# Kernel optimization log

Hardware: AMD Instinct MI355X
Metric: run time of the kernel (lower is better)

## Reference

```python
import jax, jax.numpy as jnp
import numpy as np

B, CAP, H, NH = 128, 65536, 512, 8
HD = H // NH
GH = H // 4  # gate hidden


def setup_inputs() -> dict:
    key = jax.random.key(0)
    ks = jax.random.split(key, 8)
    s = 1.0 / np.sqrt(H)
    sg = 1.0 / np.sqrt(GH)
    return {
        "query": jax.random.normal(ks[0], (B, H), jnp.float32),
        "memory_keys": jax.random.normal(ks[1], (CAP, H), jnp.float32) * s,
        "memory_values": jax.random.normal(ks[2], (CAP, H), jnp.float32) * s,
        "in_proj_w": jax.random.normal(ks[3], (3 * H, H), jnp.float32) * s,
        "in_proj_b": jnp.zeros((3 * H,), jnp.float32),
        "out_proj_w": jax.random.normal(ks[4], (H, H), jnp.float32) * s,
        "out_proj_b": jnp.zeros((H,), jnp.float32),
        "gate_w1": jax.random.normal(ks[5], (GH, H), jnp.float32) * s,
        "gate_b1": jnp.zeros((GH,), jnp.float32),
        "gate_w2": jax.random.normal(ks[6], (1, GH), jnp.float32) * sg,
        "gate_b2": jnp.zeros((1,), jnp.float32),
        "usage_count": jnp.zeros((CAP,), jnp.float32),
        "last_used": jnp.zeros((CAP,), jnp.float32),
        "step_counter": 1,
    }


def reference(query, memory_keys, memory_values, in_proj_w, in_proj_b,
              out_proj_w, out_proj_b, gate_w1, gate_b1, gate_w2, gate_b2,
              usage_count, last_used, step_counter):
    # nn.MultiheadAttention packed projections: rows [0:H]=Wq, [H:2H]=Wk, [2H:3H]=Wv
    wq, wk, wv = in_proj_w[:H], in_proj_w[H:2 * H], in_proj_w[2 * H:]
    bq, bk, bv = in_proj_b[:H], in_proj_b[H:2 * H], in_proj_b[2 * H:]

    q = (query @ wq.T + bq).reshape(B, NH, HD)           # [B, h, d] (q_len = 1)
    k = (memory_keys @ wk.T + bk).reshape(CAP, NH, HD)   # [C, h, d]
    v = (memory_values @ wv.T + bv).reshape(CAP, NH, HD)  # [C, h, d]

    scores = jnp.einsum('bhd,chd->bhc', q, k) / np.sqrt(HD)  # [B, h, C]
    attn = jax.nn.softmax(scores, axis=-1)
    ctx = jnp.einsum('bhc,chd->bhd', attn, v).reshape(B, H)
    attn_out = ctx @ out_proj_w.T + out_proj_b               # [B, H]

    # usage bookkeeping: attn_weights averaged over heads, then over batch
    avg_attn = attn.mean(axis=(0, 1))                        # [C]
    new_usage = usage_count + avg_attn
    new_last = jnp.where(avg_attn > 1e-3,
                         jnp.float32(step_counter), last_used)

    # gating MLP: Linear -> ReLU -> Linear -> Sigmoid
    gate = jax.nn.sigmoid(
        jax.nn.relu(query @ gate_w1.T + gate_b1) @ gate_w2.T + gate_b2)  # [B, 1]
    memory_output = gate * attn_out                          # [B, H]
    return memory_output, new_usage, new_last
```

## Files before the change

kernel.cpp:

```cpp
#include <hip/hip_runtime.h>
#include <stdint.h>


typedef __bf16 b16x8 __attribute__((ext_vector_type(8)));
typedef float f32x4 __attribute__((ext_vector_type(4)));

static __device__ __forceinline__ unsigned short f2bf(float f) {
  return __builtin_bit_cast(unsigned short, (__bf16)f);
}

static __device__ __forceinline__ f32x4 MFMA(b16x8 a, b16x8 b, f32x4 c) {
  return __builtin_amdgcn_mfma_f32_16x16x32_bf16(a, b, c, 0, 0, 0);
}

#define GLL16(g, l)                                                          \
  __builtin_amdgcn_global_load_lds(                                          \
      (const __attribute__((address_space(1))) void*)(g),                    \
      (__attribute__((address_space(3))) void*)(l), 16, 0, 0)

#define SBAR() __builtin_amdgcn_sched_barrier(0)

__global__ void k_convert_w(const float* __restrict__ w, unsigned short* __restrict__ dst) {
  int i = blockIdx.x * 256 + threadIdx.x;
  float4 v = reinterpret_cast<const float4*>(w + 512 * 512)[i];
  ushort4 o;
  o.x = f2bf(v.x); o.y = f2bf(v.y); o.z = f2bf(v.z); o.w = f2bf(v.w);
  reinterpret_cast<ushort4*>(dst)[i] = o;
}

__global__ void k_proj_q(const float* __restrict__ query, const float* __restrict__ w,
                         const float* __restrict__ bias, unsigned short* __restrict__ qout) {
  __shared__ float qs[512];
  int b = blockIdx.x, j = threadIdx.x;
  qs[j] = query[b * 512 + j];
  __syncthreads();
  float acc = bias[j];
  const float4* q4 = reinterpret_cast<const float4*>(qs);
  const float4* w4 = reinterpret_cast<const float4*>(w + j * 512);
#pragma unroll 8
  for (int i = 0; i < 128; ++i) {
    float4 a = q4[i], c = w4[i];
    acc += a.x * c.x + a.y * c.y + a.z * c.z + a.w * c.w;
  }
  qout[b * 512 + j] = f2bf(acc);
}

__global__ void k_gate(const float* __restrict__ query, const float* __restrict__ w1,
                       const float* __restrict__ b1, const float* __restrict__ w2,
                       const float* __restrict__ b2, float* __restrict__ gate) {
  __shared__ float qs[512];
  __shared__ float red[2];
  int b = blockIdx.x, j = threadIdx.x;
  qs[j] = query[b * 512 + j];
  qs[j + 128] = query[b * 512 + j + 128];
  qs[j + 256] = query[b * 512 + j + 256];
  qs[j + 384] = query[b * 512 + j + 384];
  __syncthreads();
  float acc = b1[j];
  const float4* q4 = reinterpret_cast<const float4*>(qs);
  const float4* w4 = reinterpret_cast<const float4*>(w1 + j * 512);
#pragma unroll 8
  for (int i = 0; i < 128; ++i) {
    float4 a = q4[i], c = w4[i];
    acc += a.x * c.x + a.y * c.y + a.z * c.z + a.w * c.w;
  }
  float t = fmaxf(acc, 0.f) * w2[j];
#pragma unroll
  for (int off = 1; off < 64; off <<= 1) t += __shfl_xor(t, off, 64);
  if ((j & 63) == 0) red[j >> 6] = t;
  __syncthreads();
  if (j == 0) {
    float z = red[0] + red[1] + b2[0];
    gate[b] = 1.f / (1.f + __builtin_amdgcn_exp2f(-z * 1.44269504088896f));
  }
}

__global__ __launch_bounds__(512, 4) void k_proj_kv(
    const float* __restrict__ mk, const float* __restrict__ mv,
    const unsigned short* __restrict__ wkb, const unsigned short* __restrict__ wvb,
    const float* __restrict__ in_b,
    unsigned short* __restrict__ kout, unsigned short* __restrict__ vtout) {
  const int p = blockIdx.x;
  const int xcd = p & 7, slot = p >> 3;
  const int isV = xcd >> 2;
  const int j0 = (slot & 3) * 128;
  const int c0 = (xcd & 3) * 16384 + (slot >> 2) * 128;
  const float* Ag = isV ? mv : mk;
  const unsigned short* W = isV ? wvb : wkb;
  const float* bias = in_b + (isV ? 1024 : 512);
  const int tid = threadIdx.x;
  const int w = tid >> 6, wr = w >> 2, wc = w & 3;
  const int ln = tid & 15, g = (tid & 63) >> 4;
  const int sw = (ln >> 1) & 3;

  __shared__ __align__(16) unsigned short Al[2][128 * 32];
  __shared__ __align__(16) unsigned short Wl[2][128 * 32];

  f32x4 acc[4][2];
#pragma unroll
  for (int m = 0; m < 4; ++m)
#pragma unroll
    for (int n = 0; n < 2; ++n) acc[m][n] = {0.f, 0.f, 0.f, 0.f};

  const int arow = tid >> 2, aq = tid & 3;
  const float* aptr = Ag + (size_t)(c0 + arow) * 512 + aq * 8;
  const int aoff = arow * 32 + ((aq ^ ((arow >> 1) & 3)) << 3);

  const int lane = tid & 63;
  const int wrow = 16 * w + (lane >> 2);
  const int wps = (lane & 3) ^ ((wrow >> 1) & 3);
  const unsigned short* wsrc = W + (size_t)(j0 + wrow) * 512 + wps * 8;
  const int wdoff = w * 512;

  float4 aA0, aA1, aB0, aB1;

  GLL16(wsrc, &Wl[0][wdoff]);
  SBAR();
  {
    const float4* ap = reinterpret_cast<const float4*>(aptr);
    aA0 = ap[0]; aA1 = ap[1];
  }
  SBAR();
  asm volatile("s_waitcnt vmcnt(0)" ::: "memory");
  SBAR();
  {
    b16x8 v;
    v[0] = (__bf16)aA0.x; v[1] = (__bf16)aA0.y; v[2] = (__bf16)aA0.z; v[3] = (__bf16)aA0.w;
    v[4] = (__bf16)aA1.x; v[5] = (__bf16)aA1.y; v[6] = (__bf16)aA1.z; v[7] = (__bf16)aA1.w;
    *reinterpret_cast<b16x8*>(&Al[0][aoff]) = v;
  }
  {
    const float4* ap = reinterpret_cast<const float4*>(aptr + 32);
    aB0 = ap[0]; aB1 = ap[1];
  }
  SBAR();
  asm volatile("s_waitcnt lgkmcnt(0)" ::: "memory");
  SBAR();
  __builtin_amdgcn_s_barrier();

#pragma unroll 2
  for (int kk = 0; kk < 16; ++kk) {
    const int cur = kk & 1, nxt = cur ^ 1;
    b16x8 af[4], wf[2];
#pragma unroll
    for (int m = 0; m < 4; ++m) {
      int row = 64 * wr + 16 * m + ln;
      af[m] = *reinterpret_cast<const b16x8*>(&Al[cur][row * 32 + ((g ^ sw) << 3)]);
    }
#pragma unroll
    for (int n = 0; n < 2; ++n) {
      int row = 32 * wc + 16 * n + ln;
      wf[n] = *reinterpret_cast<const b16x8*>(&Wl[cur][row * 32 + ((g ^ sw) << 3)]);
    }
    const int k1 = (kk < 15) ? kk + 1 : 15;
    GLL16(wsrc + k1 * 32, &Wl[nxt][wdoff]);
    SBAR();
    const int k2 = (kk < 14) ? kk + 2 : 15;
    {
      const float4* ap = reinterpret_cast<const float4*>(aptr + k2 * 32);
      if (cur == 0) { aA0 = ap[0]; aA1 = ap[1]; }
      else          { aB0 = ap[0]; aB1 = ap[1]; }
    }
    SBAR();
    if (!isV) {
#pragma unroll
      for (int m = 0; m < 4; ++m)
#pragma unroll
        for (int n = 0; n < 2; ++n) acc[m][n] = MFMA(wf[n], af[m], acc[m][n]);
    } else {
#pragma unroll
      for (int m = 0; m < 4; ++m)
#pragma unroll
        for (int n = 0; n < 2; ++n) acc[m][n] = MFMA(af[m], wf[n], acc[m][n]);
    }
    SBAR();
    asm volatile("s_waitcnt vmcnt(3)" ::: "memory");
    SBAR();
    {
      float4 f0 = (nxt == 0) ? aA0 : aB0, f1 = (nxt == 0) ? aA1 : aB1;
      b16x8 v;
      v[0] = (__bf16)f0.x; v[1] = (__bf16)f0.y; v[2] = (__bf16)f0.z; v[3] = (__bf16)f0.w;
      v[4] = (__bf16)f1.x; v[5] = (__bf16)f1.y; v[6] = (__bf16)f1.z; v[7] = (__bf16)f1.w;
      *reinterpret_cast<b16x8*>(&Al[nxt][aoff]) = v;
    }
    SBAR();
    asm volatile("s_waitcnt vmcnt(2) lgkmcnt(0)" ::: "memory");
    SBAR();
    __builtin_amdgcn_s_barrier();
  }

  if (!isV) {
#pragma unroll
    for (int m = 0; m < 4; ++m) {
      int c = c0 + 64 * wr + 16 * m + ln;
#pragma unroll
      for (int n = 0; n < 2; ++n) {
        int jb = j0 + 32 * wc + 16 * n + 4 * g;
        float4 bb = *reinterpret_cast<const float4*>(&bias[jb]);
        ushort4 o;
        o.x = f2bf(acc[m][n][0] + bb.x);
        o.y = f2bf(acc[m][n][1] + bb.y);
        o.z = f2bf(acc[m][n][2] + bb.z);
        o.w = f2bf(acc[m][n][3] + bb.w);
        *reinterpret_cast<ushort4*>(&kout[(size_t)c * 512 + jb]) = o;
      }
    }
  } else {
#pragma unroll
    for (int n = 0; n < 2; ++n) {
      int j = j0 + 32 * wc + 16 * n + ln;
      float bj = bias[j];
#pragma unroll
      for (int m = 0; m < 4; ++m) {
        int cb = c0 + 64 * wr + 16 * m + 4 * g;
        ushort4 o;
        o.x = f2bf(acc[m][n][0] + bj);
        o.y = f2bf(acc[m][n][1] + bj);
        o.z = f2bf(acc[m][n][2] + bj);
        o.w = f2bf(acc[m][n][3] + bj);
        *reinterpret_cast<ushort4*>(&vtout[(size_t)j * 65536 + cb]) = o;
      }
    }
  }
}

__global__ __launch_bounds__(256) void k_attn1(
    const unsigned short* __restrict__ kb, const unsigned short* __restrict__ vt,
    const unsigned short* __restrict__ qb,
    float* __restrict__ l_ws, float* __restrict__ ctxT) {
  const int h = blockIdx.y, cg = blockIdx.x;
  const int tid = threadIdx.x;
  const int wv = tid >> 6, wr = wv >> 1, wc = wv & 1;
  const int ln = tid & 15, g = (tid & 63) >> 4;
  __shared__ __align__(16) unsigned short kS[128 * 64];
  __shared__ __align__(16) unsigned short pS[128 * 128];
  __shared__ __align__(16) unsigned short vS[64 * 128];
  const float SC = 0.125f * 1.44269504088896f;

  b16x8 qf[4][2];
#pragma unroll
  for (int n = 0; n < 4; ++n)
#pragma unroll
    for (int ks = 0; ks < 2; ++ks) {
      int b = 64 * wc + 16 * n + ln;
      qf[n][ks] = *reinterpret_cast<const b16x8*>(&qb[(size_t)b * 512 + h * 64 + ks * 32 + g * 8]);
    }
  f32x4 pacc[2][4];
#pragma unroll
  for (int m = 0; m < 2; ++m)
#pragma unroll
    for (int n = 0; n < 4; ++n) pacc[m][n] = {0.f, 0.f, 0.f, 0.f};
  float lsum[4] = {0.f, 0.f, 0.f, 0.f};

  for (int it = 0; it < 8; ++it) {
    int c0g = cg * 1024 + it * 128;
#pragma unroll
    for (int i = 0; i < 4; ++i) {
      int fl = i * 256 + tid, row = fl >> 3, p8 = fl & 7;
      uint4 d = *reinterpret_cast<const uint4*>(&kb[(size_t)(c0g + row) * 512 + h * 64 + p8 * 8]);
      *reinterpret_cast<uint4*>(&kS[(row * 8 + (p8 ^ (row & 7))) * 8]) = d;
    }
#pragma unroll
    for (int i = 0; i < 4; ++i) {
      int fl = i * 256 + tid, row = fl >> 4, p16 = fl & 15;
      uint4 d = *reinterpret_cast<const uint4*>(&vt[(size_t)(h * 64 + row) * 65536 + c0g + p16 * 8]);
      *reinterpret_cast<uint4*>(&vS[(row * 16 + (p16 ^ (row & 7))) * 8]) = d;
    }
    __syncthreads();

    f32x4 sacc[4][4];
#pragma unroll
    for (int m = 0; m < 4; ++m)
#pragma unroll
      for (int n = 0; n < 4; ++n) sacc[m][n] = {0.f, 0.f, 0.f, 0.f};
#pragma unroll
    for (int ks = 0; ks < 2; ++ks) {
      b16x8 a[4];
#pragma unroll
      for (int m = 0; m < 4; ++m) {
        int row = 64 * wr + 16 * m + ln;
        a[m] = *reinterpret_cast<const b16x8*>(&kS[(row * 8 + ((ks * 4 + g) ^ (row & 7))) * 8]);
      }
#pragma unroll
      for (int m = 0; m < 4; ++m)
#pragma unroll
        for (int n = 0; n < 4; ++n) sacc[m][n] = MFMA(a[m], qf[n][ks], sacc[m][n]);
    }
#pragma unroll
    for (int m = 0; m < 4; ++m)
#pragma unroll
      for (int n = 0; n < 4; ++n) {
        float p0 = __builtin_amdgcn_exp2f(sacc[m][n][0] * SC);
        float p1 = __builtin_amdgcn_exp2f(sacc[m][n][1] * SC);
        float p2 = __builtin_amdgcn_exp2f(sacc[m][n][2] * SC);
        float p3 = __builtin_amdgcn_exp2f(sacc[m][n][3] * SC);
        lsum[n] += (p0 + p1) + (p2 + p3);
        int b = 64 * wc + 16 * n + ln;
        int c = 64 * wr + 16 * m + 4 * g;
        int base = b * 128 + (((c >> 3) ^ (b & 7)) * 8) + (c & 7);
        ushort2 lo, hi;
        lo.x = f2bf(p0); lo.y = f2bf(p1);
        hi.x = f2bf(p2); hi.y = f2bf(p3);
        *reinterpret_cast<ushort2*>(&pS[base]) = lo;
        *reinterpret_cast<ushort2*>(&pS[base + 2]) = hi;
      }
    __syncthreads();
#pragma unroll
    for (int ks = 0; ks < 4; ++ks) {
      b16x8 av[2], bp[4];
#pragma unroll
      for (int m = 0; m < 2; ++m) {
        int row = 32 * wr + 16 * m + ln;
        av[m] = *reinterpret_cast<const b16x8*>(&vS[(row * 16 + ((ks * 4 + g) ^ (row & 7))) * 8]);
      }
#pragma unroll
      for (int n = 0; n < 4; ++n) {
        int row = 64 * wc + 16 * n + ln;
        bp[n] = *reinterpret_cast<const b16x8*>(&pS[(row * 16 + ((ks * 4 + g) ^ (row & 7))) * 8]);
      }
#pragma unroll
      for (int m = 0; m < 2; ++m)
#pragma unroll
        for (int n = 0; n < 4; ++n) pacc[m][n] = MFMA(av[m], bp[n], pacc[m][n]);
    }
    __syncthreads();
  }
#pragma unroll
  for (int n = 0; n < 4; ++n) {
    float v = lsum[n];
    v += __shfl_xor(v, 16, 64);
    v += __shfl_xor(v, 32, 64);
    if ((tid & 63) < 16) atomicAdd(&l_ws[h * 128 + 64 * wc + 16 * n + ln], v);
  }
#pragma unroll
  for (int m = 0; m < 2; ++m)
#pragma unroll
    for (int n = 0; n < 4; ++n)
#pragma unroll
      for (int r = 0; r < 4; ++r) {
        int d = 32 * wr + 16 * m + 4 * g + r;
        int b = 64 * wc + 16 * n + ln;
        atomicAdd(&ctxT[(h * 64 + d) * 128 + b], pacc[m][n][r]);
      }
}

__global__ __launch_bounds__(256) void k_attn2(
    const unsigned short* __restrict__ kb, const unsigned short* __restrict__ qb,
    const float* __restrict__ l_ws, float* __restrict__ avgA) {
  const int h = blockIdx.y, cg = blockIdx.x;
  const int tid = threadIdx.x;
  const int wv = tid >> 6, wr = wv >> 1, wc = wv & 1;
  const int ln = tid & 15, g = (tid & 63) >> 4;
  __shared__ __align__(16) unsigned short kS[128 * 64];
  __shared__ float wS[128];
  const float SC = 0.125f * 1.44269504088896f;
  if (tid < 128) wS[tid] = 1.f / l_ws[h * 128 + tid];
  b16x8 qf[4][2];
#pragma unroll
  for (int n = 0; n < 4; ++n)
#pragma unroll
    for (int ks = 0; ks < 2; ++ks) {
      int b = 64 * wc + 16 * n + ln;
      qf[n][ks] = *reinterpret_cast<const b16x8*>(&qb[(size_t)b * 512 + h * 64 + ks * 32 + g * 8]);
    }
  __syncthreads();
  float wn[4];
#pragma unroll
  for (int n = 0; n < 4; ++n) wn[n] = wS[64 * wc + 16 * n + ln];

  for (int it = 0; it < 8; ++it) {
    int c0g = cg * 1024 + it * 128;
#pragma unroll
    for (int i = 0; i < 4; ++i) {
      int fl = i * 256 + tid, row = fl >> 3, p8 = fl & 7;
      uint4 d = *reinterpret_cast<const uint4*>(&kb[(size_t)(c0g + row) * 512 + h * 64 + p8 * 8]);
      *reinterpret_cast<uint4*>(&kS[(row * 8 + (p8 ^ (row & 7))) * 8]) = d;
    }
    __syncthreads();
    f32x4 sacc[4][4];
#pragma unroll
    for (int m = 0; m < 4; ++m)
#pragma unroll
      for (int n = 0; n < 4; ++n) sacc[m][n] = {0.f, 0.f, 0.f, 0.f};
#pragma unroll
    for (int ks = 0; ks < 2; ++ks) {
      b16x8 a[4];
#pragma unroll
      for (int m = 0; m < 4; ++m) {
        int row = 64 * wr + 16 * m + ln;
        a[m] = *reinterpret_cast<const b16x8*>(&kS[(row * 8 + ((ks * 4 + g) ^ (row & 7))) * 8]);
      }
#pragma unroll
      for (int m = 0; m < 4; ++m)
#pragma unroll
        for (int n = 0; n < 4; ++n) sacc[m][n] = MFMA(a[m], qf[n][ks], sacc[m][n]);
    }
#pragma unroll
    for (int m = 0; m < 4; ++m) {
      float s0 = 0.f, s1 = 0.f, s2 = 0.f, s3 = 0.f;
#pragma unroll
      for (int n = 0; n < 4; ++n) {
        s0 += __builtin_amdgcn_exp2f(sacc[m][n][0] * SC) * wn[n];
        s1 += __builtin_amdgcn_exp2f(sacc[m][n][1] * SC) * wn[n];
        s2 += __builtin_amdgcn_exp2f(sacc[m][n][2] * SC) * wn[n];
        s3 += __builtin_amdgcn_exp2f(sacc[m][n][3] * SC) * wn[n];
      }
#pragma unroll
      for (int off = 1; off < 16; off <<= 1) {
        s0 += __shfl_xor(s0, off, 64);
        s1 += __shfl_xor(s1, off, 64);
        s2 += __shfl_xor(s2, off, 64);
        s3 += __shfl_xor(s3, off, 64);
      }
      if (ln == 0) {
        int c = c0g + 64 * wr + 16 * m + 4 * g;
        atomicAdd(&avgA[c], s0);
        atomicAdd(&avgA[c + 1], s1);
        atomicAdd(&avgA[c + 2], s2);
        atomicAdd(&avgA[c + 3], s3);
      }
    }
    __syncthreads();
  }
}

__global__ void k_finalize(const float* __restrict__ ctxT, const float* __restrict__ l_ws,
                           const float* __restrict__ wout, const float* __restrict__ bout,
                           const float* __restrict__ gate, float* __restrict__ out) {
  __shared__ float cs[512];
  int b = blockIdx.x, j = threadIdx.x;
  cs[j] = ctxT[j * 128 + b] / l_ws[(j >> 6) * 128 + b];
  __syncthreads();
  float acc = bout[j];
  const float4* c4 = reinterpret_cast<const float4*>(cs);
  const float4* w4 = reinterpret_cast<const float4*>(wout + j * 512);
#pragma unroll 8
  for (int i = 0; i < 128; ++i) {
    float4 a = c4[i], c = w4[i];
    acc += a.x * c.x + a.y * c.y + a.z * c.z + a.w * c.w;
  }
  out[b * 512 + j] = gate[b] * acc;
}

__global__ void k_usage(const float* __restrict__ avgA, const float* __restrict__ usage,
                        const float* __restrict__ last, const int* __restrict__ step,
                        float* __restrict__ out_usage, float* __restrict__ out_last) {
  int c = blockIdx.x * 256 + threadIdx.x;
  float avg = avgA[c] * (1.f / 1024.f);
  out_usage[c] = usage[c] + avg;
  out_last[c] = (avg > 0.001f) ? (float)step[0] : last[c];
}

extern "C" void kernel_launch(void* const* d_in, const int* in_sizes, int n_in,
                              void* d_out, int out_size, void* d_ws, size_t ws_size,
                              hipStream_t stream) {
  const float* query = (const float*)d_in[0];
  const float* mk    = (const float*)d_in[1];
  const float* mv    = (const float*)d_in[2];
  const float* in_w  = (const float*)d_in[3];
  const float* in_b  = (const float*)d_in[4];
  const float* out_w = (const float*)d_in[5];
  const float* out_b = (const float*)d_in[6];
  const float* gw1   = (const float*)d_in[7];
  const float* gb1   = (const float*)d_in[8];
  const float* gw2   = (const float*)d_in[9];
  const float* gb2   = (const float*)d_in[10];
  const float* usage = (const float*)d_in[11];
  const float* last  = (const float*)d_in[12];
  const int*   step  = (const int*)d_in[13];

  char* ws = (char*)d_ws;
  unsigned short* qb  = (unsigned short*)(ws);
  unsigned short* wkb = (unsigned short*)(ws + 131072);
  unsigned short* wvb = (unsigned short*)(ws + 655360);
  unsigned short* kb  = (unsigned short*)(ws + 1179648);
  unsigned short* vt  = (unsigned short*)(ws + 68288512);
  float* l_ws = (float*)(ws + 135397376);
  float* ctxT = (float*)(ws + 135401472);
  float* avgA = (float*)(ws + 135663616);
  float* gate = (float*)(ws + 135925760);
  float* out = (float*)d_out;

  hipMemsetAsync(ws + 135397376, 0, 4096 + 262144 + 262144, stream);

  k_convert_w<<<512, 256, 0, stream>>>(in_w, wkb);
  k_proj_q<<<128, 512, 0, stream>>>(query, in_w, in_b, qb);
  k_gate<<<128, 128, 0, stream>>>(query, gw1, gb1, gw2, gb2, gate);
  k_proj_kv<<<4096, 512, 0, stream>>>(mk, mv, wkb, wvb, in_b, kb, vt);
  k_attn1<<<dim3(64, 8), 256, 0, stream>>>(kb, vt, qb, l_ws, ctxT);
  k_attn2<<<dim3(64, 8), 256, 0, stream>>>(kb, qb, l_ws, avgA);
  k_finalize<<<128, 512, 0, stream>>>(ctxT, l_ws, out_w, out_b, gate, out);
  k_usage<<<256, 256, 0, stream>>>(avgA, usage, last, step, out + 65536, out + 131072);
}
```

Before: 371.3 us.

## Load fp32 K/V tiles directly to LDS and convert at fragment read

```diff
diff --git a/kernel.cpp b/kernel.cpp
--- a/kernel.cpp
+++ b/kernel.cpp
@@ -75,7 +75,7 @@
   }
 }
 
-__global__ __launch_bounds__(512, 4) void k_proj_kv(
+__global__ __launch_bounds__(256, 2) void k_proj_kv(
     const float* __restrict__ mk, const float* __restrict__ mv,
     const unsigned short* __restrict__ wkb, const unsigned short* __restrict__ wvb,
     const float* __restrict__ in_b,
@@ -89,113 +89,104 @@
   const unsigned short* W = isV ? wvb : wkb;
   const float* bias = in_b + (isV ? 1024 : 512);
   const int tid = threadIdx.x;
-  const int w = tid >> 6, wr = w >> 2, wc = w & 3;
+  const int w = tid >> 6;
+  const int wr = w >> 1, wc = w & 1;
   const int ln = tid & 15, g = (tid & 63) >> 4;
-  const int sw = (ln >> 1) & 3;
-
-  __shared__ __align__(16) unsigned short Al[2][128 * 32];
-  __shared__ __align__(16) unsigned short Wl[2][128 * 32];
-
-  f32x4 acc[4][2];
+  const int lane = tid & 63;
+
+  __shared__ __align__(16) float          AL[3][128 * 32];
+  __shared__ __align__(16) unsigned short WL[2][128 * 32];
+
+  f32x4 acc[4][4];
 #pragma unroll
   for (int m = 0; m < 4; ++m)
 #pragma unroll
-    for (int n = 0; n < 2; ++n) acc[m][n] = {0.f, 0.f, 0.f, 0.f};
-
-  const int arow = tid >> 2, aq = tid & 3;
-  const float* aptr = Ag + (size_t)(c0 + arow) * 512 + aq * 8;
-  const int aoff = arow * 32 + ((aq ^ ((arow >> 1) & 3)) << 3);
-
-  const int lane = tid & 63;
-  const int wrow = 16 * w + (lane >> 2);
-  const int wps = (lane & 3) ^ ((wrow >> 1) & 3);
-  const unsigned short* wsrc = W + (size_t)(j0 + wrow) * 512 + wps * 8;
-  const int wdoff = w * 512;
-
-  float4 aA0, aA1, aB0, aB1;
-
-  GLL16(wsrc, &Wl[0][wdoff]);
+    for (int n = 0; n < 4; ++n) acc[m][n] = {0.f, 0.f, 0.f, 0.f};
+
+  const float* srcA[4];
+  int dstA[4];
+#pragma unroll
+  for (int i = 0; i < 4; ++i) {
+    int row = i * 32 + w * 8 + (lane >> 3);
+    int cs = (lane & 7) ^ (row & 7);
+    srcA[i] = Ag + (size_t)(c0 + row) * 512 + cs * 4;
+    dstA[i] = (i * 256 + w * 64) * 4;
+  }
+  const unsigned short* srcW[2];
+  int dstW[2];
+#pragma unroll
+  for (int i = 0; i < 2; ++i) {
+    int row = i * 64 + w * 16 + (lane >> 2);
+    int cs = (lane & 3) ^ ((row >> 1) & 3);
+    srcW[i] = W + (size_t)(j0 + row) * 512 + cs * 8;
+    dstW[i] = (i * 256 + w * 64) * 8;
+  }
+
+  GLL16(srcW[0], &WL[0][dstW[0]]);
+  GLL16(srcW[1], &WL[0][dstW[1]]);
+#pragma unroll
+  for (int i = 0; i < 4; ++i) GLL16(srcA[i], &AL[0][dstA[i]]);
+#pragma unroll
+  for (int i = 0; i < 4; ++i) GLL16(srcA[i] + 32, &AL[1][dstA[i]]);
   SBAR();
-  {
-    const float4* ap = reinterpret_cast<const float4*>(aptr);
-    aA0 = ap[0]; aA1 = ap[1];
-  }
-  SBAR();
-  asm volatile("s_waitcnt vmcnt(0)" ::: "memory");
-  SBAR();
-  {
-    b16x8 v;
-    v[0] = (__bf16)aA0.x; v[1] = (__bf16)aA0.y; v[2] = (__bf16)aA0.z; v[3] = (__bf16)aA0.w;
-    v[4] = (__bf16)aA1.x; v[5] = (__bf16)aA1.y; v[6] = (__bf16)aA1.z; v[7] = (__bf16)aA1.w;
-    *reinterpret_cast<b16x8*>(&Al[0][aoff]) = v;
-  }
-  {
-    const float4* ap = reinterpret_cast<const float4*>(aptr + 32);
-    aB0 = ap[0]; aB1 = ap[1];
-  }
-  SBAR();
-  asm volatile("s_waitcnt lgkmcnt(0)" ::: "memory");
+  asm volatile("s_waitcnt vmcnt(4)" ::: "memory");
   SBAR();
   __builtin_amdgcn_s_barrier();
-
-#pragma unroll 2
+  SBAR();
+
+#pragma unroll
   for (int kk = 0; kk < 16; ++kk) {
-    const int cur = kk & 1, nxt = cur ^ 1;
-    b16x8 af[4], wf[2];
+    const int a = kk % 3;
+    const int bwl = kk & 1;
+    const int k1 = (kk < 15) ? kk + 1 : 15;
+    const int k2 = (kk < 14) ? kk + 2 : 15;
+    GLL16(srcW[0] + k1 * 32, &WL[bwl ^ 1][dstW[0]]);
+    GLL16(srcW[1] + k1 * 32, &WL[bwl ^ 1][dstW[1]]);
+#pragma unroll
+    for (int i = 0; i < 4; ++i) GLL16(srcA[i] + k2 * 32, &AL[(kk + 2) % 3][dstA[i]]);
+    SBAR();
+    b16x8 af[4], wf[4];
 #pragma unroll
     for (int m = 0; m < 4; ++m) {
-      int row = 64 * wr + 16 * m + ln;
-      af[m] = *reinterpret_cast<const b16x8*>(&Al[cur][row * 32 + ((g ^ sw) << 3)]);
-    }
-#pragma unroll
-    for (int n = 0; n < 2; ++n) {
-      int row = 32 * wc + 16 * n + ln;
-      wf[n] = *reinterpret_cast<const b16x8*>(&Wl[cur][row * 32 + ((g ^ sw) << 3)]);
-    }
-    const int k1 = (kk < 15) ? kk + 1 : 15;
-    GLL16(wsrc + k1 * 32, &Wl[nxt][wdoff]);
+      int r = 64 * wr + 16 * m + ln;
+      f32x4 lo = *reinterpret_cast<const f32x4*>(&AL[a][r * 32 + (((2 * g) ^ (r & 7)) << 2)]);
+      f32x4 hi = *reinterpret_cast<const f32x4*>(&AL[a][r * 32 + (((2 * g + 1) ^ (r & 7)) << 2)]);
+      b16x8 v;
+      v[0] = (__bf16)lo[0]; v[1] = (__bf16)lo[1]; v[2] = (__bf16)lo[2]; v[3] = (__bf16)lo[3];
+      v[4] = (__bf16)hi[0]; v[5] = (__bf16)hi[1]; v[6] = (__bf16)hi[2]; v[7] = (__bf16)hi[3];
+      af[m] = v;
+    }
+#pragma unroll
+    for (int n = 0; n < 4; ++n) {
+      int r = 64 * wc + 16 * n + ln;
+      wf[n] = *reinterpret_cast<const b16x8*>(&WL[bwl][r * 32 + ((g ^ ((r >> 1) & 3)) << 3)]);
+    }
+    if (!isV) {
+#pragma unroll
+      for (int m = 0; m < 4; ++m)
+#pragma unroll
+        for (int n = 0; n < 4; ++n) acc[m][n] = MFMA(wf[n], af[m], acc[m][n]);
+    } else {
+#pragma unroll
+      for (int m = 0; m < 4; ++m)
+#pragma unroll
+        for (int n = 0; n < 4; ++n) acc[m][n] = MFMA(af[m], wf[n], acc[m][n]);
+    }
     SBAR();
-    const int k2 = (kk < 14) ? kk + 2 : 15;
-    {
-      const float4* ap = reinterpret_cast<const float4*>(aptr + k2 * 32);
-      if (cur == 0) { aA0 = ap[0]; aA1 = ap[1]; }
-      else          { aB0 = ap[0]; aB1 = ap[1]; }
-    }
-    SBAR();
-    if (!isV) {
-#pragma unroll
-      for (int m = 0; m < 4; ++m)
-#pragma unroll
-        for (int n = 0; n < 2; ++n) acc[m][n] = MFMA(wf[n], af[m], acc[m][n]);
-    } else {
-#pragma unroll
-      for (int m = 0; m < 4; ++m)
-#pragma unroll
-        for (int n = 0; n < 2; ++n) acc[m][n] = MFMA(af[m], wf[n], acc[m][n]);
-    }
-    SBAR();
-    asm volatile("s_waitcnt vmcnt(3)" ::: "memory");
-    SBAR();
-    {
-      float4 f0 = (nxt == 0) ? aA0 : aB0, f1 = (nxt == 0) ? aA1 : aB1;
-      b16x8 v;
-      v[0] = (__bf16)f0.x; v[1] = (__bf16)f0.y; v[2] = (__bf16)f0.z; v[3] = (__bf16)f0.w;
-      v[4] = (__bf16)f1.x; v[5] = (__bf16)f1.y; v[6] = (__bf16)f1.z; v[7] = (__bf16)f1.w;
-      *reinterpret_cast<b16x8*>(&Al[nxt][aoff]) = v;
-    }
-    SBAR();
-    asm volatile("s_waitcnt vmcnt(2) lgkmcnt(0)" ::: "memory");
+    asm volatile("s_waitcnt vmcnt(4) lgkmcnt(0)" ::: "memory");
     SBAR();
     __builtin_amdgcn_s_barrier();
-  }
+    SBAR();
+  }
+  asm volatile("s_waitcnt vmcnt(0)" ::: "memory");
 
   if (!isV) {
 #pragma unroll
     for (int m = 0; m < 4; ++m) {
       int c = c0 + 64 * wr + 16 * m + ln;
 #pragma unroll
-      for (int n = 0; n < 2; ++n) {
-        int jb = j0 + 32 * wc + 16 * n + 4 * g;
+      for (int n = 0; n < 4; ++n) {
+        int jb = j0 + 64 * wc + 16 * n + 4 * g;
         float4 bb = *reinterpret_cast<const float4*>(&bias[jb]);
         ushort4 o;
         o.x = f2bf(acc[m][n][0] + bb.x);
@@ -207,8 +198,8 @@
     }
   } else {
 #pragma unroll
-    for (int n = 0; n < 2; ++n) {
-      int j = j0 + 32 * wc + 16 * n + ln;
+    for (int n = 0; n < 4; ++n) {
+      int j = j0 + 64 * wc + 16 * n + ln;
       float bj = bias[j];
 #pragma unroll
       for (int m = 0; m < 4; ++m) {
@@ -486,7 +477,7 @@
   k_convert_w<<<512, 256, 0, stream>>>(in_w, wkb);
   k_proj_q<<<128, 512, 0, stream>>>(query, in_w, in_b, qb);
   k_gate<<<128, 128, 0, stream>>>(query, gw1, gb1, gw2, gb2, gate);
-  k_proj_kv<<<4096, 512, 0, stream>>>(mk, mv, wkb, wvb, in_b, kb, vt);
+  k_proj_kv<<<4096, 256, 0, stream>>>(mk, mv, wkb, wvb, in_b, kb, vt);
   k_attn1<<<dim3(64, 8), 256, 0, stream>>>(kb, vt, qb, l_ws, ctxT);
   k_attn2<<<dim3(64, 8), 256, 0, stream>>>(kb, qb, l_ws, avgA);
   k_finalize<<<128, 512, 0, stream>>>(ctxT, l_ws, out_w, out_b, gate, out);
```

New measurement: 371.3 us. Within noise of the previous version (+0.0%).
